# Performance work log

Hardware: AMD Instinct MI355X
Metric: run time of the kernel (lower is better)

The kernel has to match this reference:

```python
import jax, jax.numpy as jnp
import numpy as np

BETA = 0.25
K = 4096


def setup_inputs() -> dict:
    key = jax.random.key(0)
    k1, k2 = jax.random.split(key)
    z = jax.random.normal(k1, (32, 256, 32, 32), dtype=jnp.float32)
    # matches torch init: uniform(-1/k, 1/k)
    embedding = jax.random.uniform(k2, (K, 256), dtype=jnp.float32,
                                   minval=-1.0 / K, maxval=1.0 / K)
    return {"z": z, "embedding": embedding}


def reference(z, embedding):
    b, d, h, w = z.shape
    k = embedding.shape[0]
    # (b d h w) -> (n d)
    z_flat = jnp.transpose(z, (0, 2, 3, 1)).reshape(-1, d)
    # squared euclidean distances, (n, k)
    distances = (jnp.sum(z_flat * z_flat, axis=-1, keepdims=True)
                 + jnp.sum(embedding * embedding, axis=-1)
                 - 2.0 * jnp.einsum('nd,kd->nk', z_flat, embedding))
    encoding_indices = jnp.argmin(distances, axis=1)
    encodings_onehot = jax.nn.one_hot(encoding_indices, k, dtype=z.dtype)
    zq_flat = embedding[encoding_indices]
    z_quantized = jnp.transpose(zq_flat.reshape(b, h, w, d), (0, 3, 1, 2))
    loss_encoder = jnp.mean((jax.lax.stop_gradient(z_quantized) - z) ** 2)
    loss_codebook = jnp.mean((z_quantized - jax.lax.stop_gradient(z)) ** 2)
    loss = BETA * loss_encoder + loss_codebook
    # straight-through estimator
    z_quantized_st = z + jax.lax.stop_gradient(z_quantized - z)
    # perplexity of codebook usage
    enc_mean = jnp.mean(encodings_onehot, axis=0)
    perplexity = jnp.exp(-jnp.sum(enc_mean * jnp.log(enc_mean + 1e-10)))
    return (z_quantized_st, loss, perplexity, encodings_onehot,
            encoding_indices, distances)
```

## Files before the change

kernel.cpp:

```cpp
#include <hip/hip_runtime.h>
#include <hip/hip_bf16.h>

typedef unsigned short u16;
typedef unsigned int u32;
typedef unsigned long long u64;
typedef __attribute__((ext_vector_type(8))) short bf16x8;
typedef __attribute__((ext_vector_type(4))) float f32x4;

#define NROWS 32768
#define KCODES 4096
#define DDIM 256
#define HW 1024
#define ZSTRIDE_B 262144ULL

#define OFF_ZQ   0ULL
#define OFF_LOSS 8388608ULL
#define OFF_PERP 8388609ULL
#define OFF_OH   8388610ULL
#define OFF_IDX  142606338ULL
#define OFF_DIST 142639106ULL

#define T_ZH 16777280ULL
#define T_EH 25165888ULL

#define WS_IDX    0
#define WS_COUNTS 131072
#define WS_EN2    147456
#define WS_ZN2    163840
#define WS_PART   294912
#define WS_BMIN   524288

__global__ __launch_bounds__(64) void k_en2(const float* __restrict__ emb,
                                            float* __restrict__ en2) {
    int k = blockIdx.x;
    int l = threadIdx.x;
    float4 v = *(const float4*)(emb + (size_t)k * DDIM + l * 4);
    float s = v.x * v.x + v.y * v.y + v.z * v.z + v.w * v.w;
    #pragma unroll
    for (int m = 32; m; m >>= 1) s += __shfl_xor(s, m);
    if (l == 0) en2[k] = s;
}

__global__ __launch_bounds__(256) void k_zn2(const float* __restrict__ z,
                                             float* __restrict__ zn2) {
    int n = blockIdx.x * 256 + threadIdx.x;
    int b = n >> 10, hw = n & 1023;
    const float* zp = z + (size_t)b * ZSTRIDE_B + hw;
    float s = 0.f;
    #pragma unroll 8
    for (int d = 0; d < DDIM; ++d) {
        float v = zp[(size_t)d * HW];
        s = fmaf(v, v, s);
    }
    zn2[n] = s;
}

__global__ __launch_bounds__(256) void k_prep_z(const float* __restrict__ z,
                                                u16* __restrict__ Zhh) {
    __shared__ float t[32][33];
    int tx = threadIdx.x, ty = threadIdx.y;
    int h0 = blockIdx.x * 32, d0 = blockIdx.y * 32, b = blockIdx.z;
    const float* zp = z + (size_t)b * ZSTRIDE_B;
    #pragma unroll
    for (int q = 0; q < 4; ++q)
        t[ty * 4 + q][tx] = zp[(size_t)(d0 + ty * 4 + q) * HW + h0 + tx];
    __syncthreads();
    #pragma unroll
    for (int q = 0; q < 4; ++q) {
        int n = b * HW + h0 + ty * 4 + q;
        int d = d0 + tx;
        float v = t[tx][ty * 4 + q];
        __hip_bfloat16 hb = __float2bfloat16(v);
        Zhh[(size_t)n * DDIM + d] = *(u16*)&hb;
    }
}

__global__ __launch_bounds__(256) void k_prep_e(const float* __restrict__ e,
                                                u16* __restrict__ Ehh) {
    int t4 = blockIdx.x * 256 + threadIdx.x;
    float4 v = *(const float4*)(e + (size_t)t4 * 4);
    float vv[4] = {v.x, v.y, v.z, v.w};
    u16 ho[4];
    #pragma unroll
    for (int j = 0; j < 4; ++j) {
        __hip_bfloat16 hb = __float2bfloat16(vv[j]);
        ho[j] = *(u16*)&hb;
    }
    *(ushort4*)(Ehh + (size_t)t4 * 4) = make_ushort4(ho[0], ho[1], ho[2], ho[3]);
}

__global__ __launch_bounds__(256) void k_dist_mfma(
    const u16* __restrict__ Zhh, const u16* __restrict__ Ehh,
    const float* __restrict__ zn2, const float* __restrict__ en2,
    float* __restrict__ dist, float* __restrict__ bmin)
{
    __shared__ __align__(16) u16 As[4096];
    __shared__ __align__(16) u16 Bs[4096];
    const int tid = threadIdx.x;
    const int w = tid >> 6, l = tid & 63;
    const int n0 = blockIdx.x * 128, k0 = blockIdx.y * 128;
    const int kb = blockIdx.y;
    const int wr = w >> 1, wc = w & 1;

    int goff[2], loff[2];
    #pragma unroll
    for (int it = 0; it < 2; ++it) {
        int o = (w << 10) + (it << 12) + (l << 4);
        int r = o >> 6;
        int c16 = (o >> 4) & 3;
        int gs = c16 ^ ((r >> 1) & 3);
        goff[it] = r * DDIM + gs * 8;
        loff[it] = (w << 9) + (it << 11);
    }

    f32x4 acc[4][4];
    #pragma unroll
    for (int m = 0; m < 4; ++m)
        #pragma unroll
        for (int n = 0; n < 4; ++n)
            acc[m][n] = (f32x4){0.f, 0.f, 0.f, 0.f};

    const int lr = l & 15, ks = l >> 4;
    int aoff[4], boff[4];
    #pragma unroll
    for (int m = 0; m < 4; ++m) {
        int ra = wr * 64 + m * 16 + lr;
        aoff[m] = ra * 32 + (ks ^ ((ra >> 1) & 3)) * 8;
        int rb = wc * 64 + m * 16 + lr;
        boff[m] = rb * 32 + (ks ^ ((rb >> 1) & 3)) * 8;
    }

    const u16* Ap = Zhh + (size_t)n0 * DDIM;
    const u16* Bp = Ehh + (size_t)k0 * DDIM;
    for (int st = 0; st < 8; ++st) {
        const int d0 = st * 32;
        #pragma unroll
        for (int it = 0; it < 2; ++it) {
            __builtin_amdgcn_global_load_lds(
                (const __attribute__((address_space(1))) void*)(Ap + d0 + goff[it]),
                (__attribute__((address_space(3))) void*)(As + loff[it]), 16, 0, 0);
            __builtin_amdgcn_global_load_lds(
                (const __attribute__((address_space(1))) void*)(Bp + d0 + goff[it]),
                (__attribute__((address_space(3))) void*)(Bs + loff[it]), 16, 0, 0);
        }
        __syncthreads();
        bf16x8 af[4], bfr[4];
        #pragma unroll
        for (int m = 0; m < 4; ++m) af[m] = *(const bf16x8*)&As[aoff[m]];
        #pragma unroll
        for (int n = 0; n < 4; ++n) bfr[n] = *(const bf16x8*)&Bs[boff[n]];
        #pragma unroll
        for (int m = 0; m < 4; ++m)
            #pragma unroll
            for (int n = 0; n < 4; ++n)
                acc[m][n] = __builtin_amdgcn_mfma_f32_16x16x32_bf16(
                    af[m], bfr[n], acc[m][n], 0, 0, 0);
        __syncthreads();
    }

    float ev[4];
    #pragma unroll
    for (int n = 0; n < 4; ++n) ev[n] = en2[k0 + wc * 64 + n * 16 + lr];
    #pragma unroll
    for (int m = 0; m < 4; ++m) {
        #pragma unroll
        for (int r = 0; r < 4; ++r) {
            int row = n0 + wr * 64 + m * 16 + ks * 4 + r;
            float t = zn2[row];
            float* dp = dist + (size_t)row * KCODES + k0 + wc * 64 + lr;
            float rm = 3.4e38f;
            #pragma unroll
            for (int n = 0; n < 4; ++n) {
                float s  = __fadd_rn(t, ev[n]);
                float m2 = __fmul_rn(2.0f, acc[m][n][r]);
                float dv = __fsub_rn(s, m2);
                dp[n * 16] = dv;
                rm = fminf(rm, dv);
            }
            #pragma unroll
            for (int msk = 1; msk < 16; msk <<= 1)
                rm = fminf(rm, __shfl_xor(rm, msk));
            if (lr == 0)
                bmin[((size_t)row * 32 + kb) * 2 + wc] = rm;
        }
    }
}

__global__ __launch_bounds__(256) void k_select(
    const float* __restrict__ dist, const float* __restrict__ z,
    const float* __restrict__ emb, const float* __restrict__ zn2,
    const float* __restrict__ en2, const float* __restrict__ bmin,
    u32* __restrict__ idxarr)
{
    const int l = threadIdx.x & 63;
    const int row = blockIdx.x * 4 + (threadIdx.x >> 6);
    float bm = bmin[(size_t)row * 64 + l];
    float mn = bm;
    #pragma unroll
    for (int m = 1; m < 64; m <<= 1) mn = fminf(mn, __shfl_xor(mn, m));
    const float thr = mn + 1e-3f;
    u64 qual = __ballot(bm <= thr);

    const int b = row >> 10, hw = row & 1023;
    const float* zp = z + (size_t)b * ZSTRIDE_B + hw;
    float z0 = zp[(size_t)(l * 4 + 0) * HW];
    float z1 = zp[(size_t)(l * 4 + 1) * HW];
    float z2 = zp[(size_t)(l * 4 + 2) * HW];
    float z3 = zp[(size_t)(l * 4 + 3) * HW];
    const float zr = zn2[row];

    u64 best = ~0ull;
    int prev_kb = -1;
    u64 qq = qual;
    while (qq) {
        int bit = __ffsll(qq) - 1; qq &= qq - 1;
        int kb = bit >> 1;
        if (kb == prev_kb) continue;
        prev_kb = kb;
        const float* dr = dist + (size_t)row * KCODES + kb * 128;
        float2 d2 = *(const float2*)(dr + l * 2);
        u64 c0 = __ballot(d2.x <= thr);
        u64 c1 = __ballot(d2.y <= thr);
        u64 any = c0 | c1;
        while (any) {
            int src = __ffsll(any) - 1; any &= any - 1;
            #pragma unroll
            for (int e = 0; e < 2; ++e) {
                u64 msk = e ? c1 : c0;
                if (!((msk >> src) & 1)) continue;
                int k = kb * 128 + src * 2 + e;
                float4 e4 = *(const float4*)(emb + (size_t)k * DDIM + l * 4);
                float p = 0.f;
                p = fmaf(z0, e4.x, p);
                p = fmaf(z1, e4.y, p);
                p = fmaf(z2, e4.z, p);
                p = fmaf(z3, e4.w, p);
                #pragma unroll
                for (int m = 1; m < 64; m <<= 1) p += __shfl_xor(p, m);
                float dh = __fsub_rn(__fadd_rn(zr, en2[k]), __fmul_rn(2.0f, p));
                u32 ub = __float_as_uint(dh);
                ub = (ub & 0x80000000u) ? ~ub : (ub | 0x80000000u);
                u64 cand = ((u64)ub << 32) | (u32)k;
                best = cand < best ? cand : best;
            }
        }
    }
    if (l == 0) idxarr[row] = (u32)(best & 0xffffffffu);
}

__global__ __launch_bounds__(256) void k_zq(const float* __restrict__ z,
                                            const float* __restrict__ emb,
                                            const u32* __restrict__ idxarr,
                                            unsigned* __restrict__ counts,
                                            float* __restrict__ out,
                                            float* __restrict__ partials) {
    int n = blockIdx.x * 256 + threadIdx.x;
    unsigned idx = idxarr[n];
    out[OFF_IDX + n] = (float)idx;
    atomicAdd(counts + idx, 1u);
    int b = n >> 10, hw = n & 1023;
    const float* zp = z + (size_t)b * ZSTRIDE_B + hw;
    const float* ep = emb + (size_t)idx * DDIM;
    float* oq = out + OFF_ZQ + (size_t)b * ZSTRIDE_B + hw;
    float s = 0.f;
    #pragma unroll 4
    for (int d = 0; d < DDIM; ++d) {
        float ev = ep[d];
        float zv = zp[(size_t)d * HW];
        oq[(size_t)d * HW] = ev;
        float df = ev - zv;
        s = fmaf(df, df, s);
    }
    __shared__ float red[256];
    red[threadIdx.x] = s;
    __syncthreads();
    for (int st = 128; st > 0; st >>= 1) {
        if (threadIdx.x < st) red[threadIdx.x] += red[threadIdx.x + st];
        __syncthreads();
    }
    if (threadIdx.x == 0) partials[blockIdx.x] = red[0];
}

__global__ __launch_bounds__(256) void k_onehot(const u32* __restrict__ idxarr,
                                                float* __restrict__ out) {
    const int l = threadIdx.x & 63;
    const int n = blockIdx.x * 4 + (threadIdx.x >> 6);
    const int idx = (int)idxarr[n];
    float* base = out + OFF_OH + (size_t)n * KCODES;
    #pragma unroll
    for (int i = 0; i < 16; ++i) {
        int c0 = i * 256 + l * 4;
        float2 a, b2;
        a.x  = (idx == c0)     ? 1.0f : 0.0f;
        a.y  = (idx == c0 + 1) ? 1.0f : 0.0f;
        b2.x = (idx == c0 + 2) ? 1.0f : 0.0f;
        b2.y = (idx == c0 + 3) ? 1.0f : 0.0f;
        *(float2*)(base + c0) = a;
        *(float2*)(base + c0 + 2) = b2;
    }
}

__global__ __launch_bounds__(256) void k_final(const unsigned* __restrict__ counts,
                                               const float* __restrict__ partials,
                                               float* __restrict__ out) {
    __shared__ float red[256];
    int t = threadIdx.x;
    red[t] = (t < 128) ? partials[t] : 0.f;
    __syncthreads();
    for (int st = 128; st > 0; st >>= 1) {
        if (t < st) red[t] += red[t + st];
        __syncthreads();
    }
    float loss = 1.25f * (red[0] / 8388608.0f);
    __syncthreads();
    float h = 0.f;
    for (int k = t; k < KCODES; k += 256) {
        float p = (float)counts[k] * (1.0f / 32768.0f);
        h -= p * logf(p + 1e-10f);
    }
    red[t] = h;
    __syncthreads();
    for (int st = 128; st > 0; st >>= 1) {
        if (t < st) red[t] += red[t + st];
        __syncthreads();
    }
    if (t == 0) {
        out[OFF_LOSS] = loss;
        out[OFF_PERP] = expf(red[0]);
    }
}

extern "C" void kernel_launch(void* const* d_in, const int* in_sizes, int n_in,
                              void* d_out, int out_size, void* d_ws, size_t ws_size,
                              hipStream_t stream) {
    (void)in_sizes; (void)n_in; (void)out_size; (void)ws_size;
    const float* z = (const float*)d_in[0];
    const float* emb = (const float*)d_in[1];
    float* out = (float*)d_out;
    char* ws = (char*)d_ws;
    u32* idxarr = (u32*)(ws + WS_IDX);
    unsigned* counts = (unsigned*)(ws + WS_COUNTS);
    float* en2 = (float*)(ws + WS_EN2);
    float* zn2 = (float*)(ws + WS_ZN2);
    float* partials = (float*)(ws + WS_PART);
    float* bmin = (float*)(ws + WS_BMIN);

    u16* Zhh = (u16*)(out + T_ZH);
    u16* Ehh = (u16*)(out + T_EH);
    float* dist = out + OFF_DIST;

    hipMemsetAsync(counts, 0, (size_t)KCODES * 4, stream);

    k_prep_z<<<dim3(32, 8, 32), dim3(32, 8), 0, stream>>>(z, Zhh);
    k_prep_e<<<1024, 256, 0, stream>>>(emb, Ehh);
    k_en2<<<KCODES, 64, 0, stream>>>(emb, en2);
    k_zn2<<<NROWS / 256, 256, 0, stream>>>(z, zn2);
    k_dist_mfma<<<dim3(NROWS / 128, KCODES / 128), 256, 0, stream>>>(
        Zhh, Ehh, zn2, en2, dist, bmin);
    k_select<<<NROWS / 4, 256, 0, stream>>>(dist, z, emb, zn2, en2, bmin, idxarr);
    k_zq<<<NROWS / 256, 256, 0, stream>>>(z, emb, idxarr, counts, out, partials);
    k_onehot<<<NROWS / 4, 256, 0, stream>>>(idxarr, out);
    k_final<<<1, 256, 0, stream>>>(counts, partials, out);
}
```

Before: 584.6 us.

## Fuse prep kernels, deepen MFMA K-tile, reuse best distance for loss

Merges the embedding bf16 conversion into the norm kernel and vectorises the z transpose with wider tiles and float4 loads. Doubles the distance GEMM's K-slice per stage to 64 with an 8-way XOR swizzle, which halves the number of barrier rounds but doubles LDS use. The selection kernel now stores the winning distance, so the quantization kernel no longer rereads z to compute the loss. The final loss and perplexity reduction moves into block 0 of the one-hot kernel to save a launch. The loss now comes from the expanded-form distance rather than a direct difference, which may shift it slightly numerically.

```diff
diff --git a/kernel.cpp b/kernel.cpp
--- a/kernel.cpp
+++ b/kernel.cpp
@@ -28,10 +28,12 @@
 #define WS_EN2    147456
 #define WS_ZN2    163840
 #define WS_PART   294912
+#define WS_BDIST  295424
 #define WS_BMIN   524288
 
-__global__ __launch_bounds__(64) void k_en2(const float* __restrict__ emb,
-                                            float* __restrict__ en2) {
+__global__ __launch_bounds__(64) void k_prep_e_en2(const float* __restrict__ emb,
+                                                   float* __restrict__ en2,
+                                                   u16* __restrict__ Ehh) {
     int k = blockIdx.x;
     int l = threadIdx.x;
     float4 v = *(const float4*)(emb + (size_t)k * DDIM + l * 4);
@@ -39,6 +41,14 @@
     #pragma unroll
     for (int m = 32; m; m >>= 1) s += __shfl_xor(s, m);
     if (l == 0) en2[k] = s;
+    float vv[4] = {v.x, v.y, v.z, v.w};
+    u16 ho[4];
+    #pragma unroll
+    for (int j = 0; j < 4; ++j) {
+        __hip_bfloat16 hb = __float2bfloat16(vv[j]);
+        ho[j] = *(u16*)&hb;
+    }
+    *(ushort4*)(Ehh + (size_t)k * DDIM + l * 4) = make_ushort4(ho[0], ho[1], ho[2], ho[3]);
 }
 
 __global__ __launch_bounds__(256) void k_zn2(const float* __restrict__ z,
@@ -57,36 +67,37 @@
 
 __global__ __launch_bounds__(256) void k_prep_z(const float* __restrict__ z,
                                                 u16* __restrict__ Zhh) {
-    __shared__ float t[32][33];
-    int tx = threadIdx.x, ty = threadIdx.y;
-    int h0 = blockIdx.x * 32, d0 = blockIdx.y * 32, b = blockIdx.z;
+    __shared__ float t[32][132];
+    const int tid = threadIdx.x;
+    const int h0 = blockIdx.x * 128, d0 = blockIdx.y * 32, b = blockIdx.z;
     const float* zp = z + (size_t)b * ZSTRIDE_B;
-    #pragma unroll
-    for (int q = 0; q < 4; ++q)
-        t[ty * 4 + q][tx] = zp[(size_t)(d0 + ty * 4 + q) * HW + h0 + tx];
+    {
+        int hq = (tid & 31) << 2;
+        int dr = tid >> 5;
+        #pragma unroll
+        for (int p = 0; p < 4; ++p) {
+            int d = p * 8 + dr;
+            float4 v = *(const float4*)(zp + (size_t)(d0 + d) * HW + h0 + hq);
+            *(float4*)&t[d][hq] = v;
+        }
+    }
     __syncthreads();
-    #pragma unroll
-    for (int q = 0; q < 4; ++q) {
-        int n = b * HW + h0 + ty * 4 + q;
-        int d = d0 + tx;
-        float v = t[tx][ty * 4 + q];
-        __hip_bfloat16 hb = __float2bfloat16(v);
-        Zhh[(size_t)n * DDIM + d] = *(u16*)&hb;
-    }
-}
-
-__global__ __launch_bounds__(256) void k_prep_e(const float* __restrict__ e,
-                                                u16* __restrict__ Ehh) {
-    int t4 = blockIdx.x * 256 + threadIdx.x;
-    float4 v = *(const float4*)(e + (size_t)t4 * 4);
-    float vv[4] = {v.x, v.y, v.z, v.w};
-    u16 ho[4];
-    #pragma unroll
-    for (int j = 0; j < 4; ++j) {
-        __hip_bfloat16 hb = __float2bfloat16(vv[j]);
-        ho[j] = *(u16*)&hb;
-    }
-    *(ushort4*)(Ehh + (size_t)t4 * 4) = make_ushort4(ho[0], ho[1], ho[2], ho[3]);
+    {
+        int nr = tid >> 1;
+        int half = tid & 1;
+        int n = b * HW + h0 + nr;
+        u16 hv[16];
+        #pragma unroll
+        for (int i = 0; i < 16; ++i) {
+            float v = t[half * 16 + i][nr];
+            __hip_bfloat16 hb = __float2bfloat16(v);
+            hv[i] = *(u16*)&hb;
+        }
+        u16* dst = Zhh + (size_t)n * DDIM + d0 + half * 16;
+        #pragma unroll
+        for (int q = 0; q < 4; ++q)
+            *(ushort4*)(dst + q * 4) = *(ushort4*)&hv[q * 4];
+    }
 }
 
 __global__ __launch_bounds__(256) void k_dist_mfma(
@@ -94,23 +105,23 @@
     const float* __restrict__ zn2, const float* __restrict__ en2,
     float* __restrict__ dist, float* __restrict__ bmin)
 {
-    __shared__ __align__(16) u16 As[4096];
-    __shared__ __align__(16) u16 Bs[4096];
+    __shared__ __align__(16) u16 As[8192];
+    __shared__ __align__(16) u16 Bs[8192];
     const int tid = threadIdx.x;
     const int w = tid >> 6, l = tid & 63;
     const int n0 = blockIdx.x * 128, k0 = blockIdx.y * 128;
     const int kb = blockIdx.y;
     const int wr = w >> 1, wc = w & 1;
 
-    int goff[2], loff[2];
-    #pragma unroll
-    for (int it = 0; it < 2; ++it) {
-        int o = (w << 10) + (it << 12) + (l << 4);
-        int r = o >> 6;
-        int c16 = (o >> 4) & 3;
-        int gs = c16 ^ ((r >> 1) & 3);
+    int goff[4], loff[4];
+    #pragma unroll
+    for (int it = 0; it < 4; ++it) {
+        int o = (it << 12) + (w << 10) + (l << 4);
+        int r = o >> 7;
+        int c16 = (o >> 4) & 7;
+        int gs = c16 ^ (r & 7);
         goff[it] = r * DDIM + gs * 8;
-        loff[it] = (w << 9) + (it << 11);
+        loff[it] = (it << 11) + (w << 9);
     }
 
     f32x4 acc[4][4];
@@ -121,21 +132,14 @@
             acc[m][n] = (f32x4){0.f, 0.f, 0.f, 0.f};
 
     const int lr = l & 15, ks = l >> 4;
-    int aoff[4], boff[4];
-    #pragma unroll
-    for (int m = 0; m < 4; ++m) {
-        int ra = wr * 64 + m * 16 + lr;
-        aoff[m] = ra * 32 + (ks ^ ((ra >> 1) & 3)) * 8;
-        int rb = wc * 64 + m * 16 + lr;
-        boff[m] = rb * 32 + (ks ^ ((rb >> 1) & 3)) * 8;
-    }
+    const int ra = wr * 64 + lr, rb = wc * 64 + lr;
 
     const u16* Ap = Zhh + (size_t)n0 * DDIM;
     const u16* Bp = Ehh + (size_t)k0 * DDIM;
-    for (int st = 0; st < 8; ++st) {
-        const int d0 = st * 32;
-        #pragma unroll
-        for (int it = 0; it < 2; ++it) {
+    for (int st = 0; st < 4; ++st) {
+        const int d0 = st * 64;
+        #pragma unroll
+        for (int it = 0; it < 4; ++it) {
             __builtin_amdgcn_global_load_lds(
                 (const __attribute__((address_space(1))) void*)(Ap + d0 + goff[it]),
                 (__attribute__((address_space(3))) void*)(As + loff[it]), 16, 0, 0);
@@ -144,17 +148,26 @@
                 (__attribute__((address_space(3))) void*)(Bs + loff[it]), 16, 0, 0);
         }
         __syncthreads();
-        bf16x8 af[4], bfr[4];
-        #pragma unroll
-        for (int m = 0; m < 4; ++m) af[m] = *(const bf16x8*)&As[aoff[m]];
-        #pragma unroll
-        for (int n = 0; n < 4; ++n) bfr[n] = *(const bf16x8*)&Bs[boff[n]];
-        #pragma unroll
-        for (int m = 0; m < 4; ++m)
-            #pragma unroll
-            for (int n = 0; n < 4; ++n)
-                acc[m][n] = __builtin_amdgcn_mfma_f32_16x16x32_bf16(
-                    af[m], bfr[n], acc[m][n], 0, 0, 0);
+        #pragma unroll
+        for (int kk = 0; kk < 2; ++kk) {
+            bf16x8 af[4], bfr[4];
+            #pragma unroll
+            for (int m = 0; m < 4; ++m) {
+                int rr = ra + m * 16;
+                af[m] = *(const bf16x8*)&As[rr * 64 + ((kk * 4 + ks) ^ (rr & 7)) * 8];
+            }
+            #pragma unroll
+            for (int n = 0; n < 4; ++n) {
+                int rr = rb + n * 16;
+                bfr[n] = *(const bf16x8*)&Bs[rr * 64 + ((kk * 4 + ks) ^ (rr & 7)) * 8];
+            }
+            #pragma unroll
+            for (int m = 0; m < 4; ++m)
+                #pragma unroll
+                for (int n = 0; n < 4; ++n)
+                    acc[m][n] = __builtin_amdgcn_mfma_f32_16x16x32_bf16(
+                        af[m], bfr[n], acc[m][n], 0, 0, 0);
+        }
         __syncthreads();
     }
 
@@ -190,7 +203,7 @@
     const float* __restrict__ dist, const float* __restrict__ z,
     const float* __restrict__ emb, const float* __restrict__ zn2,
     const float* __restrict__ en2, const float* __restrict__ bmin,
-    u32* __restrict__ idxarr)
+    u32* __restrict__ idxarr, float* __restrict__ bdist)
 {
     const int l = threadIdx.x & 63;
     const int row = blockIdx.x * 4 + (threadIdx.x >> 6);
@@ -245,12 +258,17 @@
             }
         }
     }
-    if (l == 0) idxarr[row] = (u32)(best & 0xffffffffu);
-}
-
-__global__ __launch_bounds__(256) void k_zq(const float* __restrict__ z,
-                                            const float* __restrict__ emb,
+    if (l == 0) {
+        idxarr[row] = (u32)(best & 0xffffffffu);
+        u32 ub = (u32)(best >> 32);
+        u32 fb = (ub & 0x80000000u) ? (ub & 0x7fffffffu) : ~ub;
+        bdist[row] = __uint_as_float(fb);
+    }
+}
+
+__global__ __launch_bounds__(256) void k_zq(const float* __restrict__ emb,
                                             const u32* __restrict__ idxarr,
+                                            const float* __restrict__ bdist,
                                             unsigned* __restrict__ counts,
                                             float* __restrict__ out,
                                             float* __restrict__ partials) {
@@ -259,20 +277,13 @@
     out[OFF_IDX + n] = (float)idx;
     atomicAdd(counts + idx, 1u);
     int b = n >> 10, hw = n & 1023;
-    const float* zp = z + (size_t)b * ZSTRIDE_B + hw;
     const float* ep = emb + (size_t)idx * DDIM;
     float* oq = out + OFF_ZQ + (size_t)b * ZSTRIDE_B + hw;
-    float s = 0.f;
     #pragma unroll 4
-    for (int d = 0; d < DDIM; ++d) {
-        float ev = ep[d];
-        float zv = zp[(size_t)d * HW];
-        oq[(size_t)d * HW] = ev;
-        float df = ev - zv;
-        s = fmaf(df, df, s);
-    }
+    for (int d = 0; d < DDIM; ++d)
+        oq[(size_t)d * HW] = ep[d];
     __shared__ float red[256];
-    red[threadIdx.x] = s;
+    red[threadIdx.x] = bdist[n];
     __syncthreads();
     for (int st = 128; st > 0; st >>= 1) {
         if (threadIdx.x < st) red[threadIdx.x] += red[threadIdx.x + st];
@@ -282,6 +293,8 @@
 }
 
 __global__ __launch_bounds__(256) void k_onehot(const u32* __restrict__ idxarr,
+                                                const unsigned* __restrict__ counts,
+                                                const float* __restrict__ partials,
                                                 float* __restrict__ out) {
     const int l = threadIdx.x & 63;
     const int n = blockIdx.x * 4 + (threadIdx.x >> 6);
@@ -298,35 +311,32 @@
         *(float2*)(base + c0) = a;
         *(float2*)(base + c0 + 2) = b2;
     }
-}
-
-__global__ __launch_bounds__(256) void k_final(const unsigned* __restrict__ counts,
-                                               const float* __restrict__ partials,
-                                               float* __restrict__ out) {
-    __shared__ float red[256];
-    int t = threadIdx.x;
-    red[t] = (t < 128) ? partials[t] : 0.f;
-    __syncthreads();
-    for (int st = 128; st > 0; st >>= 1) {
-        if (t < st) red[t] += red[t + st];
-        __syncthreads();
-    }
-    float loss = 1.25f * (red[0] / 8388608.0f);
-    __syncthreads();
-    float h = 0.f;
-    for (int k = t; k < KCODES; k += 256) {
-        float p = (float)counts[k] * (1.0f / 32768.0f);
-        h -= p * logf(p + 1e-10f);
-    }
-    red[t] = h;
-    __syncthreads();
-    for (int st = 128; st > 0; st >>= 1) {
-        if (t < st) red[t] += red[t + st];
-        __syncthreads();
-    }
-    if (t == 0) {
-        out[OFF_LOSS] = loss;
-        out[OFF_PERP] = expf(red[0]);
+    if (blockIdx.x == 0) {
+        __shared__ float red[256];
+        int t = threadIdx.x;
+        red[t] = (t < 128) ? partials[t] : 0.f;
+        __syncthreads();
+        for (int st = 128; st > 0; st >>= 1) {
+            if (t < st) red[t] += red[t + st];
+            __syncthreads();
+        }
+        float loss = 1.25f * (red[0] / 8388608.0f);
+        __syncthreads();
+        float h = 0.f;
+        for (int k = t; k < KCODES; k += 256) {
+            float p = (float)counts[k] * (1.0f / 32768.0f);
+            h -= p * logf(p + 1e-10f);
+        }
+        red[t] = h;
+        __syncthreads();
+        for (int st = 128; st > 0; st >>= 1) {
+            if (t < st) red[t] += red[t + st];
+            __syncthreads();
+        }
+        if (t == 0) {
+            out[OFF_LOSS] = loss;
+            out[OFF_PERP] = expf(red[0]);
+        }
     }
 }
 
@@ -343,6 +353,7 @@
     float* en2 = (float*)(ws + WS_EN2);
     float* zn2 = (float*)(ws + WS_ZN2);
     float* partials = (float*)(ws + WS_PART);
+    float* bdist = (float*)(ws + WS_BDIST);
     float* bmin = (float*)(ws + WS_BMIN);
 
     u16* Zhh = (u16*)(out + T_ZH);
@@ -351,14 +362,13 @@
 
     hipMemsetAsync(counts, 0, (size_t)KCODES * 4, stream);
 
-    k_prep_z<<<dim3(32, 8, 32), dim3(32, 8), 0, stream>>>(z, Zhh);
-    k_prep_e<<<1024, 256, 0, stream>>>(emb, Ehh);
-    k_en2<<<KCODES, 64, 0, stream>>>(emb, en2);
+    k_prep_z<<<dim3(8, 8, 32), 256, 0, stream>>>(z, Zhh);
+    k_prep_e_en2<<<KCODES, 64, 0, stream>>>(emb, en2, Ehh);
     k_zn2<<<NROWS / 256, 256, 0, stream>>>(z, zn2);
     k_dist_mfma<<<dim3(NROWS / 128, KCODES / 128), 256, 0, stream>>>(
         Zhh, Ehh, zn2, en2, dist, bmin);
-    k_select<<<NROWS / 4, 256, 0, stream>>>(dist, z, emb, zn2, en2, bmin, idxarr);
-    k_zq<<<NROWS / 256, 256, 0, stream>>>(z, emb, idxarr, counts, out, partials);
-    k_onehot<<<NROWS / 4, 256, 0, stream>>>(idxarr, out);
-    k_final<<<1, 256, 0, stream>>>(counts, partials, out);
-}
+    k_select<<<NROWS / 4, 256, 0, stream>>>(dist, z, emb, zn2, en2, bmin,
+                                            idxarr, bdist);
+    k_zq<<<NROWS / 256, 256, 0, stream>>>(emb, idxarr, bdist, counts, out, partials);
+    k_onehot<<<NROWS / 4, 256, 0, stream>>>(idxarr, counts, partials, out);
+}
```

Result: faster. 566.3 us (-3.1%).
